# Kernel optimization log

Hardware: AMD Instinct MI355X
Metric: run time of the kernel (lower is better)

## Reference

```python
import jax, jax.numpy as jnp
import numpy as np
import math

# normalizer: the module takes it as a callable; we use a standard smooth
# inverse-norm normalizer 1/sqrt(x^2 + eps) applied to the e_inf-like component.
_EPS = 1e-3

def _normalizer(x):
    return 1.0 / jnp.sqrt(x * x + _EPS)


def _dist_vec(tri, basis):
    # tri: (B,H,N,C,5); basis: (5,5,6)
    # vec[...,z] = sum_{x,y} basis[x,y,z] * tri_n[...,x] * tri_n[...,y]
    tri_n = tri * _normalizer(tri[..., 4:5])
    return jnp.einsum('xyz,bhncx,bhncy->bhncz', basis, tri_n, tri_n)


def setup_inputs() -> dict:
    key = jax.random.key(0)
    ks = jax.random.split(key, 8)
    B, H, N, C, S = 1, 8, 4096, 8, 16
    return {
        'q_mv': jax.random.normal(ks[0], (B, H, N, C, 32), jnp.float32),
        'k_mv': jax.random.normal(ks[1], (B, H, N, C, 32), jnp.float32),
        'v_mv': jax.random.normal(ks[2], (B, H, N, C, 32), jnp.float32),
        'q_s': jax.random.normal(ks[3], (B, H, N, S), jnp.float32),
        'k_s': jax.random.normal(ks[4], (B, H, N, S), jnp.float32),
        'v_s': jax.random.normal(ks[5], (B, H, N, S), jnp.float32),
        'basis_q': jax.random.normal(ks[6], (5, 5, 6), jnp.float32),
        'basis_k': jax.random.normal(ks[7], (5, 5, 6), jnp.float32),
    }


def reference(q_mv, k_mv, v_mv, q_s, k_s, v_s, basis_q, basis_k):
    B, H, N, C_qk, _ = q_mv.shape
    C_v = v_mv.shape[-2]
    S_qk = q_s.shape[-1]
    S_v = v_s.shape[-1]
    NUM_IP = 30   # len(_INNER_PRODUCT_WO_EXTREMES_IDX) = indices 1..30
    NUM_DIST = 6
    n_qk = C_qk * (NUM_IP + NUM_DIST) + S_qk
    n_v = C_v * 32 + S_v
    n_ch = 8 * (-(-max(n_qk, n_v) // 8))  # round up to multiple of 8

    # grade-1 components -> distance features
    q_dist = _dist_vec(q_mv[..., 1:6], basis_q)  # (B,H,N,C,6)
    k_dist = _dist_vec(k_mv[..., 1:6], basis_k)

    # inner-product components (indices 1..30)
    q_ip = q_mv[..., 1:31].reshape(B, H, N, C_qk * NUM_IP)
    k_ip = k_mv[..., 1:31].reshape(B, H, N, C_qk * NUM_IP)

    zpad_qk = jnp.zeros((B, H, N, n_ch - n_qk), q_mv.dtype)
    zpad_v = jnp.zeros((B, H, N, n_ch - n_v), v_mv.dtype)

    q = jnp.concatenate([q_ip, q_dist.reshape(B, H, N, -1), q_s, zpad_qk], -1)
    k = jnp.concatenate([k_ip, k_dist.reshape(B, H, N, -1), k_s, zpad_qk], -1)
    v = jnp.concatenate([v_mv.reshape(B, H, N, C_v * 32), v_s, zpad_v], -1)
    k = k * math.sqrt(n_ch / n_qk)

    # standard scaled dot-product attention with scale 1/sqrt(n_ch)
    scale = 1.0 / math.sqrt(n_ch)
    scores = jnp.einsum('bhqd,bhkd->bhqk', q, k) * scale
    attn = jax.nn.softmax(scores, axis=-1)
    v_out = jnp.einsum('bhqk,bhkd->bhqd', attn, v)

    v_out_mv = v_out[..., :C_v * 32].reshape(B, H, N, C_v, 32)
    v_out_s = v_out[..., C_v * 32:C_v * 32 + S_v]
    return (v_out_mv, v_out_s)
```

## Files before the change

kernel.cpp:

```cpp
#include <hip/hip_runtime.h>
#include <math.h>

typedef short bf16x8 __attribute__((ext_vector_type(8)));
typedef float f32x4 __attribute__((ext_vector_type(4)));
typedef int   i32x4 __attribute__((ext_vector_type(4)));

#define HH 8
#define NN 4096
#define DIP 256
#define DDX 256
#define DKM 192
#define DV 272
#define BN 64
#define NT (NN/BN)

typedef const __attribute__((address_space(1))) unsigned int* gp_t;
typedef __attribute__((address_space(3))) unsigned int* lp_t;
__device__ __forceinline__ void gload16(const void* g, void* l) {
    __builtin_amdgcn_global_load_lds((gp_t)g, (lp_t)l, 16, 0, 0);
}

__device__ __forceinline__ unsigned short f2bf(float f) {
    unsigned int u = __float_as_uint(f);
    u = (u + 0x7fffu + ((u >> 16) & 1u)) >> 16;
    return (unsigned short)u;
}
__device__ __forceinline__ float bf2f(unsigned short h) {
    return __uint_as_float(((unsigned int)h) << 16);
}
__device__ __forceinline__ float fexp2(float x) {
    float r;
    asm("v_exp_f32 %0, %1" : "=v"(r) : "v"(x));
    return r;
}
__device__ __forceinline__ signed char q8(float x) {
    int v = __float2int_rn(x * 21.1666667f);
    v = v < -127 ? -127 : (v > 127 ? 127 : v);
    return (signed char)v;
}

#define MFMA16(A,B,C) __builtin_amdgcn_mfma_f32_16x16x32_bf16((A),(B),(C),0,0,0)
#define MFMAI8(A,B,C) __builtin_amdgcn_mfma_i32_16x16x64_i8((A),(B),(C),0,0,0)

__global__ void feat_kernel(const float* __restrict__ mv,
                            const float* __restrict__ sv,
                            const float* __restrict__ basis,
                            float scale, int qmode,
                            signed char* __restrict__ fip,
                            unsigned short* __restrict__ fdx)
{
    __shared__ float sb[150];
    int t = threadIdx.x;
    if (t < 150) sb[t] = basis[t];
    __syncthreads();
    int row = blockIdx.x * 32 + (t >> 3);
    int c = t & 7;
    const float* m = mv + (size_t)row * 256 + c * 32;
    float f[32];
    #pragma unroll
    for (int i = 0; i < 8; ++i) {
        float4 v = ((const float4*)m)[i];
        f[i*4+0] = v.x; f[i*4+1] = v.y; f[i*4+2] = v.z; f[i*4+3] = v.w;
    }
    signed char* ip = fip + (size_t)row * DIP;
    unsigned short* dx = fdx + (size_t)row * (qmode ? DDX : DKM);
    #pragma unroll
    for (int j = 0; j < 30; ++j)
        ip[c*30 + j] = q8(f[1+j]);
    if (c < 2) {
        #pragma unroll
        for (int i = 0; i < 8; ++i)
            ip[240 + c*8 + i] = q8(sv[(size_t)row*16 + c*8 + i]);
    }
    float nn = 1.0f / sqrtf(f[5]*f[5] + 0.001f);
    float tn[5];
    #pragma unroll
    for (int x = 0; x < 5; ++x) tn[x] = f[1+x] * nn;
    #pragma unroll
    for (int z = 0; z < 6; ++z) {
        float acc = 0.f;
        #pragma unroll
        for (int x = 0; x < 5; ++x) {
            #pragma unroll
            for (int y = 0; y < 5; ++y)
                acc = fmaf(sb[(x*5+y)*6 + z] * tn[x], tn[y], acc);
        }
        acc *= scale;
        unsigned short hi = f2bf(acc);
        float r1 = acc - bf2f(hi);
        unsigned short mi = f2bf(r1);
        float r2 = r1 - bf2f(mi);
        unsigned short lo = f2bf(r2);
        int cz = c*6 + z;
        if (qmode) {
            dx[cz]      = hi;  dx[48 + cz]  = hi;
            dx[96 + cz] = mi;  dx[144 + cz] = lo;
            if (cz < 16) { dx[208 + cz] = 0; dx[240 + cz] = 0; }
            if (cz >= 32) { dx[160 + cz] = mi; dx[192 + cz] = hi; }
        } else {
            dx[cz]      = mi;  dx[48 + cz]  = lo;
            dx[96 + cz] = hi;  dx[144 + cz] = hi;
        }
    }
}

__global__ void vtrans_kernel(const float* __restrict__ vmv,
                              const float* __restrict__ vs,
                              unsigned short* __restrict__ dst)
{
    __shared__ unsigned short tile[64][DV];
    int blk = blockIdx.x;
    int h = blk >> 6;
    int n0 = (blk & 63) << 6;
    int t = threadIdx.x;
    #pragma unroll
    for (int it = 0; it < 16; ++it) {
        int v = t + it*256;
        int r = v >> 6;
        int sg = v & 63;
        float4 x = *(const float4*)(vmv + ((size_t)(h*NN + n0 + r))*256 + sg*4);
        tile[r][sg*4+0] = f2bf(x.x);
        tile[r][sg*4+1] = f2bf(x.y);
        tile[r][sg*4+2] = f2bf(x.z);
        tile[r][sg*4+3] = f2bf(x.w);
    }
    #pragma unroll
    for (int it = 0; it < 4; ++it) {
        int v = t + it*256;
        int r = v >> 4;
        int si = v & 15;
        tile[r][256 + si] = f2bf(vs[((size_t)(h*NN + n0 + r))*16 + si]);
    }
    __syncthreads();
    #pragma unroll
    for (int it = 0; it < 17; ++it) {
        int v = t + it*256;
        int dd = v >> 4;
        int sg = v & 15;
        ushort4 o;
        o.x = tile[sg*4+0][dd];
        o.y = tile[sg*4+1][dd];
        o.z = tile[sg*4+2][dd];
        o.w = tile[sg*4+3][dd];
        *(ushort4*)(dst + ((size_t)(h*DV + dd))*NN + n0 + sg*4) = o;
    }
}

__global__ __launch_bounds__(512, 1)
void attn_kernel(const signed char*    __restrict__ Qip,
                 const unsigned short* __restrict__ Qdx,
                 const signed char*    __restrict__ Kip,
                 const unsigned short* __restrict__ Kmx,
                 const unsigned short* __restrict__ Vt,
                 float* __restrict__ out)
{
    __shared__ __align__(128) unsigned short smem[66560];

    int blk = blockIdx.x;
    int sbk = ((blk & 7) << 5) | (blk >> 3);
    int h = sbk >> 5;
    int q0 = (sbk & 31) * 128;
    int tid = threadIdx.x;
    int w = tid >> 6;
    int lane = tid & 63;
    int l15 = lane & 15;
    int l4 = lane >> 4;
    int l7l = l15 & 3;
    int l7h = (l15 >> 2) & 1;
    int x7 = l15 & 7;

    const signed char* qipr = Qip + (size_t)(h*NN + q0 + w*16 + l15) * DIP + l4*16;
    i32x4 qip[4];
    #pragma unroll
    for (int s = 0; s < 4; ++s) qip[s] = *(const i32x4*)(qipr + s*64);
    const unsigned short* qdxr = Qdx + (size_t)(h*NN + q0 + w*16 + l15) * DDX + l4*8;
    bf16x8 qdx[8];
    #pragma unroll
    for (int ks = 0; ks < 8; ++ks) qdx[ks] = *(const bf16x8*)(qdxr + ks*32);

    int cl16 = (l4 ^ l7l) * 16;
    int mA  = l15*384 + cl16 + l7h*64;
    int mB  = l15*384 + cl16 + 64 - l7h*64;
    int kti[4];
    #pragma unroll
    for (int s = 0; s < 4; ++s)
        kti[s] = l15*256 + (((s*4 + l4) ^ x7) << 4);
    int vb0 = (l15>>1)*256 + ((((l15&1)*8 + l4) ^ (l15>>1)) << 4);
    int vb1 = (l15>>1)*256 + ((((l15&1)*8 + 4 + l4) ^ (l15>>1)) << 4);
    int pbW = 116736 + w*2048 + l15*128;
    int pw[4];
    #pragma unroll
    for (int kt4 = 0; kt4 < 4; ++kt4)
        pw[kt4] = pbW + (((kt4*2 + (l4>>1)) ^ x7) << 4) + ((l4&1) << 3);
    int pr0 = pbW + ((l4 ^ x7) << 4);
    int pr1 = pbW + (((4+l4) ^ x7) << 4);

    int kts0, kts1;
    { int idx = tid;       int r_ = idx>>4, sg_ = idx&15; kts0 = r_*256 + ((sg_ ^ (r_&7))<<4); }
    { int idx = tid+512;   int r_ = idx>>4, sg_ = idx&15; kts1 = r_*256 + ((sg_ ^ (r_&7))<<4); }
    int kms0, kms1, kms2;
#define KMFL(SLOT, DST) { int r_ = (SLOT)/24, fp_ = (SLOT)%24; \
    int g_ = fp_>>3, po_ = fp_&7; \
    int pl_ = ((((po_>>2)&1) ^ ((r_>>2)&1)) << 2) | ((po_&3) ^ (r_&3)); \
    DST = r_*DKM + (g_*8 + pl_)*8; }
    KMFL(tid, kms0) KMFL(tid+512, kms1) KMFL(tid+1024, kms2)
#undef KMFL
    int vts0, vts1, vts2, vts3, vts4;
#define VTF(SLOT, DST) { int ch_ = (SLOT)>>4, ps_ = (SLOT)&15; int ls_ = ps_ ^ (ch_&7); \
    DST = (ch_*2 + (ls_>>3))*NN + (ls_&7)*8; }
    VTF(tid, vts0) VTF(tid+512, vts1) VTF(tid+1024, vts2) VTF(tid+1536, vts3) VTF(tid+2048, vts4)
#undef VTF

    const signed char*    kiph = Kip + (size_t)h*NN*DIP;
    const unsigned short* kmxh = Kmx + (size_t)h*NN*DKM;
    const unsigned short* vh   = Vt  + (size_t)h*DV*NN;

    f32x4 zero = {0.f, 0.f, 0.f, 0.f};
    i32x4 zi = {0, 0, 0, 0};
    f32x4 oacc[17];
    #pragma unroll
    for (int ct = 0; ct < 17; ++ct) oacc[ct] = zero;
    float mreg = -__builtin_inff();
    float lreg = 0.f;
    const float F = 0.08274443827037988f * (6.0f/127.0f) * (6.0f/127.0f);

#define ISSUE_K(TILE, BUF) do { \
    const signed char* ks_ = kiph + (size_t)(TILE)*BN*DIP; \
    const unsigned short* ms_ = kmxh + (size_t)(TILE)*BN*DKM; \
    char* ktd_ = (char*)smem + (BUF)*16384; \
    char* kmd_ = (char*)smem + 32768 + (BUF)*24576; \
    gload16(ks_ + kts0, ktd_ + tid*16); \
    gload16(ks_ + kts1, ktd_ + (tid+512)*16); \
    gload16(ms_ + kms0, kmd_ + tid*16); \
    gload16(ms_ + kms1, kmd_ + (tid+512)*16); \
    gload16(ms_ + kms2, kmd_ + (tid+1024)*16); \
} while (0)

#define ISSUE_V(TILE) do { \
    const unsigned short* vs_ = vh + (TILE)*BN; \
    char* vtd_ = (char*)smem + 81920; \
    gload16(vs_ + vts0, vtd_ + tid*16); \
    gload16(vs_ + vts1, vtd_ + (tid+512)*16); \
    gload16(vs_ + vts2, vtd_ + (tid+1024)*16); \
    gload16(vs_ + vts3, vtd_ + (tid+1536)*16); \
    if (tid < 128) gload16(vs_ + vts4, vtd_ + (tid+2048)*16); \
} while (0)

    ISSUE_K(0, 0);
    int cur = 0;
    #pragma unroll 1
    for (int t = 0; t < NT; ++t) {
        ISSUE_V(t);
        if (t < NT-1) {
            ISSUE_K(t+1, cur^1);
            if (w < 2) asm volatile("s_waitcnt vmcnt(10)" ::: "memory");
            else       asm volatile("s_waitcnt vmcnt(9)"  ::: "memory");
        } else {
            if (w < 2) asm volatile("s_waitcnt vmcnt(5)" ::: "memory");
            else       asm volatile("s_waitcnt vmcnt(4)" ::: "memory");
        }
        __builtin_amdgcn_sched_barrier(0);
        __builtin_amdgcn_s_barrier();
        __builtin_amdgcn_sched_barrier(0);

        const char* ktb = (const char*)smem + cur*16384;
        const char* kmb = (const char*)smem + 32768 + cur*24576;

        f32x4 sf[4];
        i32x4 si[4];
        __builtin_amdgcn_s_setprio(1);
        #pragma unroll
        for (int kt4 = 0; kt4 < 4; ++kt4) {
            const char* kb = ktb + kt4*4096;
            i32x4 a = zi;
            a = MFMAI8(*(const i32x4*)(kb + kti[0]), qip[0], a);
            a = MFMAI8(*(const i32x4*)(kb + kti[1]), qip[1], a);
            a = MFMAI8(*(const i32x4*)(kb + kti[2]), qip[2], a);
            a = MFMAI8(*(const i32x4*)(kb + kti[3]), qip[3], a);
            si[kt4] = a;
            const char* kk = kmb + kt4*6144;
            bf16x8 ka0 = *(const bf16x8*)(kk + mA);
            bf16x8 ka1 = *(const bf16x8*)(kk + mB);
            bf16x8 ka2 = *(const bf16x8*)(kk + mA + 128);
            bf16x8 kb0 = *(const bf16x8*)(kk + mB + 128);
            bf16x8 kb1 = *(const bf16x8*)(kk + mA + 256);
            bf16x8 kb2 = *(const bf16x8*)(kk + mB + 256);
            f32x4 d = zero;
            d = MFMA16(ka0, qdx[0], d);
            d = MFMA16(ka1, qdx[1], d);
            d = MFMA16(ka2, qdx[2], d);
            d = MFMA16(kb0, qdx[3], d);
            d = MFMA16(kb1, qdx[4], d);
            d = MFMA16(kb2, qdx[5], d);
            d = MFMA16(ka0, qdx[3], d);
            d = MFMA16(ka1, qdx[6], d);
            d = MFMA16(kb0, qdx[0], d);
            d = MFMA16(kb1, qdx[7], d);
            sf[kt4] = d;
        }
        __builtin_amdgcn_s_setprio(0);

        f32x4 sn[4];
        #pragma unroll
        for (int kt4 = 0; kt4 < 4; ++kt4) {
            sn[kt4][0] = sf[kt4][0] + F * (float)si[kt4][0];
            sn[kt4][1] = sf[kt4][1] + F * (float)si[kt4][1];
            sn[kt4][2] = sf[kt4][2] + F * (float)si[kt4][2];
            sn[kt4][3] = sf[kt4][3] + F * (float)si[kt4][3];
        }

        float pm = fmaxf(
            fmaxf(fmaxf(fmaxf(sn[0][0], sn[0][1]), fmaxf(sn[0][2], sn[0][3])),
                  fmaxf(fmaxf(sn[1][0], sn[1][1]), fmaxf(sn[1][2], sn[1][3]))),
            fmaxf(fmaxf(fmaxf(sn[2][0], sn[2][1]), fmaxf(sn[2][2], sn[2][3])),
                  fmaxf(fmaxf(sn[3][0], sn[3][1]), fmaxf(sn[3][2], sn[3][3]))));
        pm = fmaxf(pm, __shfl_xor(pm, 16, 64));
        pm = fmaxf(pm, __shfl_xor(pm, 32, 64));
        if (!__all(pm <= mreg + 8.0f)) {
            float mnew = fmaxf(mreg, pm);
            float al = fexp2(mreg - mnew);
            mreg = mnew;
            lreg *= al;
            float a0 = __shfl(al, l4*4+0, 64);
            float a1 = __shfl(al, l4*4+1, 64);
            float a2 = __shfl(al, l4*4+2, 64);
            float a3 = __shfl(al, l4*4+3, 64);
            #pragma unroll
            for (int ct = 0; ct < 17; ++ct) {
                oacc[ct][0] *= a0; oacc[ct][1] *= a1;
                oacc[ct][2] *= a2; oacc[ct][3] *= a3;
            }
        }
        char* pbp = (char*)smem;
        #pragma unroll
        for (int kt4 = 0; kt4 < 4; ++kt4) {
            float p0 = fexp2(sn[kt4][0] - mreg), p1 = fexp2(sn[kt4][1] - mreg);
            float p2 = fexp2(sn[kt4][2] - mreg), p3 = fexp2(sn[kt4][3] - mreg);
            lreg += (p0 + p1) + (p2 + p3);
            unsigned r01, r23;
            asm("v_cvt_pk_bf16_f32 %0, %1, %2" : "=v"(r01) : "v"(p0), "v"(p1));
            asm("v_cvt_pk_bf16_f32 %0, %1, %2" : "=v"(r23) : "v"(p2), "v"(p3));
            unsigned long long pk = ((unsigned long long)r23 << 32) | (unsigned long long)r01;
            *(unsigned long long*)(pbp + pw[kt4]) = pk;
        }

        if (t < NT-1) asm volatile("s_waitcnt vmcnt(5)" ::: "memory");
        else          asm volatile("s_waitcnt vmcnt(0)" ::: "memory");
        __builtin_amdgcn_sched_barrier(0);
        __builtin_amdgcn_s_barrier();
        __builtin_amdgcn_sched_barrier(0);

        {
            bf16x8 pa0 = *(const bf16x8*)(pbp + pr0);
            bf16x8 pa1 = *(const bf16x8*)(pbp + pr1);
            const char* vtb = (const char*)smem + 81920;
            __builtin_amdgcn_s_setprio(1);
            #pragma unroll
            for (int ct = 0; ct < 17; ++ct) {
                bf16x8 bv0 = *(const bf16x8*)(vtb + ct*2048 + vb0);
                oacc[ct] = MFMA16(pa0, bv0, oacc[ct]);
            }
            #pragma unroll
            for (int ct = 0; ct < 17; ++ct) {
                bf16x8 bv1 = *(const bf16x8*)(vtb + ct*2048 + vb1);
                oacc[ct] = MFMA16(pa1, bv1, oacc[ct]);
            }
            __builtin_amdgcn_s_setprio(0);
        }
        __builtin_amdgcn_s_barrier();
        __builtin_amdgcn_sched_barrier(0);
        cur ^= 1;
    }
#undef ISSUE_K
#undef ISSUE_V

    float lf = lreg;
    lf += __shfl_xor(lf, 16, 64);
    lf += __shfl_xor(lf, 32, 64);
    const size_t mv_total = (size_t)HH * NN * 256;
    #pragma unroll
    for (int j = 0; j < 4; ++j) {
        float inv = 1.0f / __shfl(lf, l4*4 + j, 64);
        int q = q0 + w*16 + l4*4 + j;
        float* po = out + ((size_t)h*NN + q) * 256 + l15;
        #pragma unroll
        for (int ct = 0; ct < 16; ++ct)
            po[ct*16] = oacc[ct][j] * inv;
        out[mv_total + ((size_t)h*NN + q)*16 + l15] = oacc[16][j] * inv;
    }
}

extern "C" void kernel_launch(void* const* d_in, const int* in_sizes, int n_in,
                              void* d_out, int out_size, void* d_ws, size_t ws_size,
                              hipStream_t stream)
{
    const float* q_mv = (const float*)d_in[0];
    const float* k_mv = (const float*)d_in[1];
    const float* v_mv = (const float*)d_in[2];
    const float* q_s  = (const float*)d_in[3];
    const float* k_s  = (const float*)d_in[4];
    const float* v_s  = (const float*)d_in[5];
    const float* basis_q = (const float*)d_in[6];
    const float* basis_k = (const float*)d_in[7];
    float* out = (float*)d_out;

    signed char* qip8 = (signed char*)d_ws;
    signed char* kip8 = qip8 + (size_t)HH*NN*DIP;
    unsigned short* qdx = (unsigned short*)(kip8 + (size_t)HH*NN*DIP);
    unsigned short* kmx = qdx + (size_t)HH*NN*DDX;
    unsigned short* vt  = kmx + (size_t)HH*NN*DKM;

    const float qscale = 0.08274443827037988f;

    feat_kernel<<<dim3(1024), dim3(256), 0, stream>>>(q_mv, q_s, basis_q, qscale, 1, qip8, qdx);
    feat_kernel<<<dim3(1024), dim3(256), 0, stream>>>(k_mv, k_s, basis_k, 1.0f,   0, kip8, kmx);
    vtrans_kernel<<<dim3(512), dim3(256), 0, stream>>>(v_mv, v_s, vt);
    attn_kernel<<<dim3(256), dim3(512), 0, stream>>>(qip8, qdx, kip8, kmx, vt, out);
}
```

Baseline: 258.2 us.

## Split PV output columns across paired waves to share V fragment loads

Each wave now computes the PV product for its own 16 query rows and for its partner wave's rows (w^4), but only over half of the 17 value column tiles. Each V fragment read from LDS then feeds two query-row blocks, roughly halving V LDS traffic per MFMA. The partner's rescale factor and final row sums are exchanged through extra shared memory, which adds an LDS wait, one more barrier at the end, and uneven work between the two halves (9 versus 8 tiles).

```diff
diff --git a/kernel.cpp b/kernel.cpp
--- a/kernel.cpp
+++ b/kernel.cpp
@@ -154,7 +154,7 @@
                  const unsigned short* __restrict__ Vt,
                  float* __restrict__ out)
 {
-    __shared__ __align__(128) unsigned short smem[66560];
+    __shared__ __align__(128) unsigned short smem[67072];
 
     int blk = blockIdx.x;
     int sbk = ((blk & 7) << 5) | (blk >> 3);
@@ -162,6 +162,8 @@
     int q0 = (sbk & 31) * 128;
     int tid = threadIdx.x;
     int w = tid >> 6;
+    int wp = w ^ 4;
+    int kh = w >> 2;
     int lane = tid & 63;
     int l15 = lane & 15;
     int l4 = lane >> 4;
@@ -188,12 +190,19 @@
     int vb0 = (l15>>1)*256 + ((((l15&1)*8 + l4) ^ (l15>>1)) << 4);
     int vb1 = (l15>>1)*256 + ((((l15&1)*8 + 4 + l4) ^ (l15>>1)) << 4);
     int pbW = 116736 + w*2048 + l15*128;
+    int pbP = 116736 + wp*2048 + l15*128;
     int pw[4];
     #pragma unroll
     for (int kt4 = 0; kt4 < 4; ++kt4)
         pw[kt4] = pbW + (((kt4*2 + (l4>>1)) ^ x7) << 4) + ((l4&1) << 3);
-    int pr0 = pbW + ((l4 ^ x7) << 4);
-    int pr1 = pbW + (((4+l4) ^ x7) << 4);
+    int prO0 = pbW + ((l4 ^ x7) << 4);
+    int prO1 = pbW + (((4+l4) ^ x7) << 4);
+    int prP0 = pbP + ((l4 ^ x7) << 4);
+    int prP1 = pbP + (((4+l4) ^ x7) << 4);
+    int awr = 133120 + w*64 + l15*4;
+    int ard = 133120 + wp*64 + l4*16;
+    int lwr = 133632 + w*64 + l15*4;
+    int lrd = 133632 + wp*64 + l4*16;
 
     int kts0, kts1;
     { int idx = tid;       int r_ = idx>>4, sg_ = idx&15; kts0 = r_*256 + ((sg_ ^ (r_&7))<<4); }
@@ -217,9 +226,9 @@
 
     f32x4 zero = {0.f, 0.f, 0.f, 0.f};
     i32x4 zi = {0, 0, 0, 0};
-    f32x4 oacc[17];
-    #pragma unroll
-    for (int ct = 0; ct < 17; ++ct) oacc[ct] = zero;
+    f32x4 oacc[9][2];
+    #pragma unroll
+    for (int i = 0; i < 9; ++i) { oacc[i][0] = zero; oacc[i][1] = zero; }
     float mreg = -__builtin_inff();
     float lreg = 0.f;
     const float F = 0.08274443827037988f * (6.0f/127.0f) * (6.0f/127.0f);
@@ -316,9 +325,10 @@
                   fmaxf(fmaxf(sn[3][0], sn[3][1]), fmaxf(sn[3][2], sn[3][3]))));
         pm = fmaxf(pm, __shfl_xor(pm, 16, 64));
         pm = fmaxf(pm, __shfl_xor(pm, 32, 64));
+        float al = 1.0f;
         if (!__all(pm <= mreg + 8.0f)) {
             float mnew = fmaxf(mreg, pm);
-            float al = fexp2(mreg - mnew);
+            al = fexp2(mreg - mnew);
             mreg = mnew;
             lreg *= al;
             float a0 = __shfl(al, l4*4+0, 64);
@@ -326,12 +336,13 @@
             float a2 = __shfl(al, l4*4+2, 64);
             float a3 = __shfl(al, l4*4+3, 64);
             #pragma unroll
-            for (int ct = 0; ct < 17; ++ct) {
-                oacc[ct][0] *= a0; oacc[ct][1] *= a1;
-                oacc[ct][2] *= a2; oacc[ct][3] *= a3;
+            for (int i = 0; i < 9; ++i) {
+                oacc[i][0][0] *= a0; oacc[i][0][1] *= a1;
+                oacc[i][0][2] *= a2; oacc[i][0][3] *= a3;
             }
         }
         char* pbp = (char*)smem;
+        if (l4 == 0) *(float*)(pbp + awr) = al;
         #pragma unroll
         for (int kt4 = 0; kt4 < 4; ++kt4) {
             float p0 = fexp2(sn[kt4][0] - mreg), p1 = fexp2(sn[kt4][1] - mreg);
@@ -344,6 +355,7 @@
             *(unsigned long long*)(pbp + pw[kt4]) = pk;
         }
 
+        asm volatile("s_waitcnt lgkmcnt(0)" ::: "memory");
         if (t < NT-1) asm volatile("s_waitcnt vmcnt(5)" ::: "memory");
         else          asm volatile("s_waitcnt vmcnt(0)" ::: "memory");
         __builtin_amdgcn_sched_barrier(0);
@@ -351,19 +363,29 @@
         __builtin_amdgcn_sched_barrier(0);
 
         {
-            bf16x8 pa0 = *(const bf16x8*)(pbp + pr0);
-            bf16x8 pa1 = *(const bf16x8*)(pbp + pr1);
+            f32x4 ap = *(const f32x4*)(pbp + ard);
+            #pragma unroll
+            for (int i = 0; i < 9; ++i) {
+                oacc[i][1][0] *= ap[0]; oacc[i][1][1] *= ap[1];
+                oacc[i][1][2] *= ap[2]; oacc[i][1][3] *= ap[3];
+            }
+            bf16x8 paO0 = *(const bf16x8*)(pbp + prO0);
+            bf16x8 paO1 = *(const bf16x8*)(pbp + prO1);
+            bf16x8 paP0 = *(const bf16x8*)(pbp + prP0);
+            bf16x8 paP1 = *(const bf16x8*)(pbp + prP1);
             const char* vtb = (const char*)smem + 81920;
             __builtin_amdgcn_s_setprio(1);
             #pragma unroll
-            for (int ct = 0; ct < 17; ++ct) {
-                bf16x8 bv0 = *(const bf16x8*)(vtb + ct*2048 + vb0);
-                oacc[ct] = MFMA16(pa0, bv0, oacc[ct]);
-            }
-            #pragma unroll
-            for (int ct = 0; ct < 17; ++ct) {
-                bf16x8 bv1 = *(const bf16x8*)(vtb + ct*2048 + vb1);
-                oacc[ct] = MFMA16(pa1, bv1, oacc[ct]);
+            for (int i = 0; i < 9; ++i) {
+                if (i < 8 || kh == 0) {
+                    int ct = kh*9 + i;
+                    bf16x8 bv0 = *(const bf16x8*)(vtb + ct*2048 + vb0);
+                    bf16x8 bv1 = *(const bf16x8*)(vtb + ct*2048 + vb1);
+                    oacc[i][0] = MFMA16(paO0, bv0, oacc[i][0]);
+                    oacc[i][0] = MFMA16(paO1, bv1, oacc[i][0]);
+                    oacc[i][1] = MFMA16(paP0, bv0, oacc[i][1]);
+                    oacc[i][1] = MFMA16(paP1, bv1, oacc[i][1]);
+                }
             }
             __builtin_amdgcn_s_setprio(0);
         }
@@ -377,16 +399,36 @@
     float lf = lreg;
     lf += __shfl_xor(lf, 16, 64);
     lf += __shfl_xor(lf, 32, 64);
+    char* pbp = (char*)smem;
+    if (l4 == 0) *(float*)(pbp + lwr) = lf;
+    asm volatile("s_waitcnt lgkmcnt(0)" ::: "memory");
+    __builtin_amdgcn_sched_barrier(0);
+    __builtin_amdgcn_s_barrier();
+    __builtin_amdgcn_sched_barrier(0);
+    f32x4 lp = *(const f32x4*)(pbp + lrd);
+
     const size_t mv_total = (size_t)HH * NN * 256;
     #pragma unroll
     for (int j = 0; j < 4; ++j) {
-        float inv = 1.0f / __shfl(lf, l4*4 + j, 64);
-        int q = q0 + w*16 + l4*4 + j;
-        float* po = out + ((size_t)h*NN + q) * 256 + l15;
-        #pragma unroll
-        for (int ct = 0; ct < 16; ++ct)
-            po[ct*16] = oacc[ct][j] * inv;
-        out[mv_total + ((size_t)h*NN + q)*16 + l15] = oacc[16][j] * inv;
+        float invO = 1.0f / __shfl(lf, l4*4 + j, 64);
+        float invP = 1.0f / lp[j];
+        int qO = q0 + w*16 + l4*4 + j;
+        int qP = q0 + wp*16 + l4*4 + j;
+        float* poO = out + ((size_t)h*NN + qO) * 256 + l15;
+        float* poP = out + ((size_t)h*NN + qP) * 256 + l15;
+        #pragma unroll
+        for (int i = 0; i < 9; ++i) {
+            if (i < 8 || kh == 0) {
+                int ct = kh*9 + i;
+                if (ct < 16) {
+                    poO[ct*16] = oacc[i][0][j] * invO;
+                    poP[ct*16] = oacc[i][1][j] * invP;
+                } else {
+                    out[mv_total + ((size_t)h*NN + qO)*16 + l15] = oacc[i][0][j] * invO;
+                    out[mv_total + ((size_t)h*NN + qP)*16 + l15] = oacc[i][1][j] * invP;
+                }
+            }
+        }
     }
 }
 
```

New measurement: 260.8 us. Within noise of the previous version (+1.0%).
